# Performance work log

Hardware: AMD Instinct MI355X
Metric: run time of the kernel (lower is better)

Reference implementation:

```python
import jax, jax.numpy as jnp
import numpy as np
from jax import lax

C = 512
BN_EPS = 1e-5
GLN_EPS = 1e-8


def setup_inputs() -> dict:
    key = jax.random.key(0)
    ks = jax.random.split(key, 10)
    B, T = 16, 4000
    x = jax.random.normal(ks[0], (B, C, T), dtype=jnp.float32)
    # BatchNorm1d params (eval mode: affine + running stats)
    bn_gamma = jax.random.normal(ks[1], (C,), dtype=jnp.float32) * 0.1 + 1.0
    bn_beta = jax.random.normal(ks[2], (C,), dtype=jnp.float32) * 0.1
    bn_mean = jax.random.normal(ks[3], (C,), dtype=jnp.float32) * 0.1
    bn_var = jax.random.uniform(ks[4], (C,), dtype=jnp.float32) + 0.5
    # depthwise Conv1d(512,512,3,groups=512,bias=False): kernel [O=C, I=1, K=3]
    dw_w = jax.random.normal(ks[5], (C, 1, 3), dtype=jnp.float32) * (1.0 / np.sqrt(3.0))
    # PReLU default: single shared parameter init 0.25
    prelu_a = jnp.full((1,), 0.25, dtype=jnp.float32)
    # GlobalLayerNorm(512) affine params
    gln_gamma = jnp.ones((C,), dtype=jnp.float32)
    gln_beta = jnp.zeros((C,), dtype=jnp.float32)
    # pointwise Conv1d(512,512,1,bias=False): weight [O, I]
    pw_w = jax.random.normal(ks[6], (C, C), dtype=jnp.float32) * (1.0 / np.sqrt(C))
    return {"x": x, "bn_gamma": bn_gamma, "bn_beta": bn_beta, "bn_mean": bn_mean,
            "bn_var": bn_var, "dw_w": dw_w, "prelu_a": prelu_a,
            "gln_gamma": gln_gamma, "gln_beta": gln_beta, "pw_w": pw_w}


def reference(x, bn_gamma, bn_beta, bn_mean, bn_var, dw_w, prelu_a,
              gln_gamma, gln_beta, pw_w):
    # ReLU
    h = jax.nn.relu(x)
    # BatchNorm1d (eval mode, running stats), per-channel affine over [B,C,T]
    scale = (bn_gamma * lax.rsqrt(bn_var + BN_EPS))[None, :, None]
    h = h * scale + (bn_beta - bn_mean * bn_gamma * lax.rsqrt(bn_var + BN_EPS))[None, :, None]
    # depthwise conv1d, kernel 3, pad 1, groups=C
    h = lax.conv_general_dilated(h, dw_w, window_strides=(1,), padding=((1, 1),),
                                 feature_group_count=C,
                                 dimension_numbers=("NCH", "OIH", "NCH"))
    # PReLU (single shared slope)
    h = jnp.where(h >= 0, h, prelu_a[0] * h)
    # GlobalLayerNorm: normalize over (C, T) per sample, per-channel affine
    mean = jnp.mean(h, axis=(1, 2), keepdims=True)
    var = jnp.mean(jnp.square(h - mean), axis=(1, 2), keepdims=True)
    h = gln_gamma[None, :, None] * (h - mean) * lax.rsqrt(var + GLN_EPS) + gln_beta[None, :, None]
    # pointwise 1x1 conv == channel GEMM
    h = jnp.einsum("oc,bct->bot", pw_w, h)
    # residual
    return h + x
```

## Files before the change

kernel.cpp:

```cpp
#include <hip/hip_runtime.h>
#include <stdint.h>

#define B_ 16
#define C_ 512
#define T_ 4000
#define TPAD 4096

typedef float f32x4 __attribute__((ext_vector_type(4)));
typedef __bf16 bf16x8 __attribute__((ext_vector_type(8)));

__device__ inline unsigned short f2b(float f) {
  uint32_t u = __builtin_bit_cast(uint32_t, f);
  u = (u + 0x7fffu + ((u >> 16) & 1u)) >> 16;
  return (unsigned short)u;
}
__device__ inline float b2f(unsigned short h) {
  uint32_t u = ((uint32_t)h) << 16;
  return __builtin_bit_cast(float, u);
}
__device__ inline void gl_lds16(const void* g, void* s) {
  __builtin_amdgcn_global_load_lds(
      (const __attribute__((address_space(1))) uint32_t*)g,
      (__attribute__((address_space(3))) uint32_t*)s, 16, 0, 0);
}


__global__ void k_init(float* wsf) {
  int i = threadIdx.x;
  if (i < 32) wsf[i] = 0.f;
}

__global__ __launch_bounds__(64) void k_prepw(const float* __restrict__ pw,
                                              const float* __restrict__ gamma,
                                              const float* __restrict__ beta,
                                              unsigned short* __restrict__ Wp,
                                              float* __restrict__ wsf) {
  int o = blockIdx.x, l = threadIdx.x;
  float a1 = 0.f, a2 = 0.f;
  for (int j = 0; j < 8; ++j) {
    int c = j * 64 + l;
    float wv = pw[o * 512 + c];
    unsigned short wb = f2b(wv * gamma[c]);
    Wp[o * 512 + c] = wb;
    a1 += b2f(wb);
    a2 += wv * beta[c];
  }
  for (int s = 32; s > 0; s >>= 1) { a1 += __shfl_down(a1, s); a2 += __shfl_down(a2, s); }
  if (l == 0) { wsf[64 + o] = a1; wsf[576 + o] = a2; }
}

__global__ __launch_bounds__(512) void k_front(const float* __restrict__ x,
    const float* __restrict__ bng, const float* __restrict__ bnb,
    const float* __restrict__ bnm, const float* __restrict__ bnv,
    const float* __restrict__ dw, const float* __restrict__ pa,
    unsigned short* __restrict__ hT, float* __restrict__ wsf) {
  __shared__ unsigned short hs[256 * 128] __attribute__((aligned(16)));
  __shared__ float psc[128], pbi[128], pq0[128], pq1[128], pq2[128];
  __shared__ float partial[16];
  int tid = threadIdx.x;
  int l = tid & 63, w = tid >> 6;
  int tb = blockIdx.x;
  int cb = blockIdx.y;
  int b  = blockIdx.z;
  int t0 = tb * 256;
  if (tid < 128) {
    int c = cb * 128 + tid;
    float sc = bng[c] * rsqrtf(bnv[c] + 1e-5f);
    psc[tid] = sc;
    pbi[tid] = bnb[c] - bnm[c] * sc;
    pq0[tid] = dw[3 * c];
    pq1[tid] = dw[3 * c + 1];
    pq2[tid] = dw[3 * c + 2];
  }
  float alpha = pa[0];
  __syncthreads();

  int t = t0 + 4 * l;
  bool full = (t + 3 < T_);
  bool has_l = (t0 > 0);
  bool has_r = (t0 + 256 < T_);
  float sum = 0.f, sq = 0.f;
  int cs_x = (l & 7) << 3;

#pragma unroll 2
  for (int i = 0; i < 16; ++i) {
    int cl = w * 16 + i;
    const float* xr = x + ((size_t)b * C_ + cb * 128 + cl) * T_;
    float sc = psc[cl], bi = pbi[cl];
    float w0 = pq0[cl], w1 = pq1[cl], w2 = pq2[cl];
    f32x4 u;
    if (full) {
      const f32x4 v = *(const f32x4*)(xr + t);
      u.x = fmaxf(v.x, 0.f) * sc + bi;
      u.y = fmaxf(v.y, 0.f) * sc + bi;
      u.z = fmaxf(v.z, 0.f) * sc + bi;
      u.w = fmaxf(v.w, 0.f) * sc + bi;
    } else {
      u = (f32x4){0.f, 0.f, 0.f, 0.f};
    }
    float el = has_l ? (fmaxf(xr[t0 - 1], 0.f) * sc + bi) : 0.f;
    float er = has_r ? (fmaxf(xr[t0 + 256], 0.f) * sc + bi) : 0.f;
    float up = __shfl_up(u.w, 1);   if (l == 0)  up = el;
    float un = __shfl_down(u.x, 1); if (l == 63) un = er;
    float h[4];
    h[0] = w0 * up  + w1 * u.x + w2 * u.y;
    h[1] = w0 * u.x + w1 * u.y + w2 * u.z;
    h[2] = w0 * u.y + w1 * u.z + w2 * u.w;
    h[3] = w0 * u.z + w1 * u.w + w2 * un;
    int cs = cl ^ cs_x;
#pragma unroll
    for (int j = 0; j < 4; ++j) {
      float p = h[j] >= 0.f ? h[j] : alpha * h[j];
      if (!full) p = 0.f;
      sum += p; sq += p * p;
      hs[(4 * l + j) * 128 + cs] = f2b(p);
    }
  }

  for (int s = 32; s > 0; s >>= 1) { sum += __shfl_down(sum, s); sq += __shfl_down(sq, s); }
  if (l == 0) { partial[w] = sum; partial[8 + w] = sq; }
  __syncthreads();
  if (tid == 0) {
    float a = 0.f, c2 = 0.f;
    for (int k = 0; k < 8; ++k) { a += partial[k]; c2 += partial[8 + k]; }
    atomicAdd(&wsf[b], a);
    atomicAdd(&wsf[16 + b], c2);
  }

  unsigned short* dstb = hT + ((size_t)b * TPAD + t0) * 512 + cb * 128;
#pragma unroll
  for (int p = 0; p < 8; ++p) {
    int idx = p * 512 + tid;
    int tl = idx >> 4, g = idx & 15;
    int gs = g ^ ((tl >> 2) & 7);
    uint4 val = *(const uint4*)(hs + tl * 128 + gs * 8);
    *(uint4*)(dstb + (size_t)tl * 512 + g * 8) = val;
  }
}

__global__ void k_finalize(float* wsf) {
  int b = threadIdx.x;
  if (b < 16) {
    float n = (float)C_ * (float)T_;
    float mean = wsf[b] / n;
    float var = wsf[16 + b] / n - mean * mean;
    wsf[32 + b] = mean;
    wsf[48 + b] = rsqrtf(fmaxf(var, 0.f) + 1e-8f);
  }
}

__global__ __launch_bounds__(256) void k_gemm(const unsigned short* __restrict__ Wp,
    const unsigned short* __restrict__ hT, const float* __restrict__ x,
    const float* __restrict__ wsf, float* __restrict__ out) {
  __shared__ unsigned short As[128 * 64];
  __shared__ unsigned short Bs[128 * 64];
  int tid = threadIdx.x;
  int l = tid & 63, w = tid >> 6;
  int nb = blockIdx.x, mb = blockIdx.y, b = blockIdx.z;
  int wm = w >> 1, wn = w & 1;
  const unsigned short* hTb = hT + (size_t)b * TPAD * 512;

  int aoff[4], boff[4];
#pragma unroll
  for (int r = 0; r < 4; ++r) {
    int i = r * 256 + tid;
    int row = i >> 3, s = i & 7;
    int ksl = (s ^ (row & 7)) << 3;
    aoff[r] = (mb * 128 + row) * 512 + ksl;
    boff[r] = (nb * 128 + row) * 512 + ksl;
  }

  f32x4 acc[4][4] = {};
  for (int ks = 0; ks < 8; ++ks) {
    int kofs = ks * 64;
#pragma unroll
    for (int r = 0; r < 4; ++r) {
      int i = r * 256 + tid;
      gl_lds16(Wp + aoff[r] + kofs, As + i * 8);
      gl_lds16(hTb + boff[r] + kofs, Bs + i * 8);
    }
    __syncthreads();
#pragma unroll
    for (int kk = 0; kk < 2; ++kk) {
      bf16x8 af[4], bfr[4];
#pragma unroll
      for (int fm = 0; fm < 4; ++fm) {
        int row = wm * 64 + fm * 16 + (l & 15);
        int slot = ((l >> 4) + kk * 4) ^ (row & 7);
        af[fm] = *(const bf16x8*)(As + row * 64 + slot * 8);
      }
#pragma unroll
      for (int fn = 0; fn < 4; ++fn) {
        int row = wn * 64 + fn * 16 + (l & 15);
        int slot = ((l >> 4) + kk * 4) ^ (row & 7);
        bfr[fn] = *(const bf16x8*)(Bs + row * 64 + slot * 8);
      }
#pragma unroll
      for (int fm = 0; fm < 4; ++fm)
#pragma unroll
        for (int fn = 0; fn < 4; ++fn)
          acc[fm][fn] = __builtin_amdgcn_mfma_f32_16x16x32_bf16(af[fm], bfr[fn], acc[fm][fn], 0, 0, 0);
    }
    __syncthreads();
  }

  float mean = wsf[32 + b], rstd = wsf[48 + b];
  float mr = mean * rstd;
#pragma unroll
  for (int fm = 0; fm < 4; ++fm) {
    int o0 = mb * 128 + wm * 64 + fm * 16 + ((l >> 4) << 2);
    float bias[4];
#pragma unroll
    for (int j = 0; j < 4; ++j) {
      int o = o0 + j;
      bias[j] = wsf[576 + o] - mr * wsf[64 + o];
    }
#pragma unroll
    for (int fn = 0; fn < 4; ++fn) {
      int t = nb * 128 + wn * 64 + fn * 16 + (l & 15);
      if (t < T_) {
#pragma unroll
        for (int j = 0; j < 4; ++j) {
          int o = o0 + j;
          size_t idx = ((size_t)b * C_ + o) * T_ + t;
          out[idx] = rstd * acc[fm][fn][j] + bias[j] + x[idx];
        }
      }
    }
  }
}

extern "C" void kernel_launch(void* const* d_in, const int* in_sizes, int n_in,
                              void* d_out, int out_size, void* d_ws, size_t ws_size,
                              hipStream_t stream) {
  const float* x   = (const float*)d_in[0];
  const float* bng = (const float*)d_in[1];
  const float* bnb = (const float*)d_in[2];
  const float* bnm = (const float*)d_in[3];
  const float* bnv = (const float*)d_in[4];
  const float* dw  = (const float*)d_in[5];
  const float* pa  = (const float*)d_in[6];
  const float* gg  = (const float*)d_in[7];
  const float* gb  = (const float*)d_in[8];
  const float* pw  = (const float*)d_in[9];
  float* out = (float*)d_out;
  float* wsf = (float*)d_ws;
  unsigned short* Wp = (unsigned short*)((char*)d_ws + 8192);
  unsigned short* hT = (unsigned short*)((char*)d_ws + (1 << 20));

  k_init<<<dim3(1), dim3(64), 0, stream>>>(wsf);
  k_prepw<<<dim3(512), dim3(64), 0, stream>>>(pw, gg, gb, Wp, wsf);
  k_front<<<dim3(16, 4, 16), dim3(512), 0, stream>>>(x, bng, bnb, bnm, bnv, dw, pa, hT, wsf);
  k_finalize<<<dim3(1), dim3(64), 0, stream>>>(wsf);
  k_gemm<<<dim3(32, 4, 16), dim3(256), 0, stream>>>(Wp, hT, x, wsf, out);
}
```

Baseline: 156.4 us.

## Double-buffer GEMM LDS tiles with 256x256 blocks and 8 waves

After: 153.9 us. No clear change (-1.6%).

```diff
diff --git a/kernel.cpp b/kernel.cpp
--- a/kernel.cpp
+++ b/kernel.cpp
@@ -149,66 +149,84 @@
   }
 }
 
-__global__ __launch_bounds__(256) void k_gemm(const unsigned short* __restrict__ Wp,
+__global__ __launch_bounds__(512, 2) void k_gemm(const unsigned short* __restrict__ Wp,
     const unsigned short* __restrict__ hT, const float* __restrict__ x,
     const float* __restrict__ wsf, float* __restrict__ out) {
-  __shared__ unsigned short As[128 * 64];
-  __shared__ unsigned short Bs[128 * 64];
+  __shared__ unsigned short As0[8192], As1[8192], Bs0[8192], Bs1[8192];
   int tid = threadIdx.x;
   int l = tid & 63, w = tid >> 6;
   int nb = blockIdx.x, mb = blockIdx.y, b = blockIdx.z;
-  int wm = w >> 1, wn = w & 1;
+  int wm = w >> 2, wn = w & 3;
   const unsigned short* hTb = hT + (size_t)b * TPAD * 512;
 
-  int aoff[4], boff[4];
-#pragma unroll
-  for (int r = 0; r < 4; ++r) {
-    int i = r * 256 + tid;
-    int row = i >> 3, s = i & 7;
-    int ksl = (s ^ (row & 7)) << 3;
-    aoff[r] = (mb * 128 + row) * 512 + ksl;
-    boff[r] = (nb * 128 + row) * 512 + ksl;
-  }
-
-  f32x4 acc[4][4] = {};
-  for (int ks = 0; ks < 8; ++ks) {
-    int kofs = ks * 64;
-#pragma unroll
-    for (int r = 0; r < 4; ++r) {
-      int i = r * 256 + tid;
-      gl_lds16(Wp + aoff[r] + kofs, As + i * 8);
-      gl_lds16(hTb + boff[r] + kofs, Bs + i * 8);
-    }
+  int aoff[2], boff[2], ldso[2];
+#pragma unroll
+  for (int r = 0; r < 2; ++r) {
+    int i = r * 512 + tid;
+    int row = i >> 2, s = i & 3;
+    int ksl = (s ^ ((row >> 1) & 3)) << 3;
+    aoff[r] = (mb * 256 + row) * 512 + ksl;
+    boff[r] = (nb * 256 + row) * 512 + ksl;
+    ldso[r] = i * 8;
+  }
+
+  int aro[8], bro[4];
+#pragma unroll
+  for (int fm = 0; fm < 8; ++fm) {
+    int row = wm * 128 + fm * 16 + (l & 15);
+    int slot = (l >> 4) ^ ((row >> 1) & 3);
+    aro[fm] = row * 32 + slot * 8;
+  }
+#pragma unroll
+  for (int fn = 0; fn < 4; ++fn) {
+    int row = wn * 64 + fn * 16 + (l & 15);
+    int slot = (l >> 4) ^ ((row >> 1) & 3);
+    bro[fn] = row * 32 + slot * 8;
+  }
+
+  const unsigned short *cA = As0, *cB = Bs0;
+  unsigned short *nA = As1, *nB = Bs1;
+
+#pragma unroll
+  for (int r = 0; r < 2; ++r) {
+    gl_lds16(Wp + aoff[r], As0 + ldso[r]);
+    gl_lds16(hTb + boff[r], Bs0 + ldso[r]);
+  }
+  __syncthreads();
+
+  f32x4 acc[8][4] = {};
+#pragma unroll 1
+  for (int kt = 0; kt < 16; ++kt) {
+    if (kt < 15) {
+      int kofs = (kt + 1) * 32;
+#pragma unroll
+      for (int r = 0; r < 2; ++r) {
+        gl_lds16(Wp + aoff[r] + kofs, nA + ldso[r]);
+        gl_lds16(hTb + boff[r] + kofs, nB + ldso[r]);
+      }
+    }
+    bf16x8 af[8], bfv[4];
+#pragma unroll
+    for (int fm = 0; fm < 8; ++fm) af[fm] = *(const bf16x8*)(cA + aro[fm]);
+#pragma unroll
+    for (int fn = 0; fn < 4; ++fn) bfv[fn] = *(const bf16x8*)(cB + bro[fn]);
+    __builtin_amdgcn_s_setprio(1);
+#pragma unroll
+    for (int fm = 0; fm < 8; ++fm)
+#pragma unroll
+      for (int fn = 0; fn < 4; ++fn)
+        acc[fm][fn] = __builtin_amdgcn_mfma_f32_16x16x32_bf16(af[fm], bfv[fn], acc[fm][fn], 0, 0, 0);
+    __builtin_amdgcn_s_setprio(0);
     __syncthreads();
-#pragma unroll
-    for (int kk = 0; kk < 2; ++kk) {
-      bf16x8 af[4], bfr[4];
-#pragma unroll
-      for (int fm = 0; fm < 4; ++fm) {
-        int row = wm * 64 + fm * 16 + (l & 15);
-        int slot = ((l >> 4) + kk * 4) ^ (row & 7);
-        af[fm] = *(const bf16x8*)(As + row * 64 + slot * 8);
-      }
-#pragma unroll
-      for (int fn = 0; fn < 4; ++fn) {
-        int row = wn * 64 + fn * 16 + (l & 15);
-        int slot = ((l >> 4) + kk * 4) ^ (row & 7);
-        bfr[fn] = *(const bf16x8*)(Bs + row * 64 + slot * 8);
-      }
-#pragma unroll
-      for (int fm = 0; fm < 4; ++fm)
-#pragma unroll
-        for (int fn = 0; fn < 4; ++fn)
-          acc[fm][fn] = __builtin_amdgcn_mfma_f32_16x16x32_bf16(af[fm], bfr[fn], acc[fm][fn], 0, 0, 0);
-    }
-    __syncthreads();
+    const unsigned short* t1 = cA; cA = nA; nA = (unsigned short*)t1;
+    const unsigned short* t2 = cB; cB = nB; nB = (unsigned short*)t2;
   }
 
   float mean = wsf[32 + b], rstd = wsf[48 + b];
   float mr = mean * rstd;
 #pragma unroll
-  for (int fm = 0; fm < 4; ++fm) {
-    int o0 = mb * 128 + wm * 64 + fm * 16 + ((l >> 4) << 2);
+  for (int fm = 0; fm < 8; ++fm) {
+    int o0 = mb * 256 + wm * 128 + fm * 16 + ((l >> 4) << 2);
     float bias[4];
 #pragma unroll
     for (int j = 0; j < 4; ++j) {
@@ -217,7 +235,7 @@
     }
 #pragma unroll
     for (int fn = 0; fn < 4; ++fn) {
-      int t = nb * 128 + wn * 64 + fn * 16 + (l & 15);
+      int t = nb * 256 + wn * 64 + fn * 16 + (l & 15);
       if (t < T_) {
 #pragma unroll
         for (int j = 0; j < 4; ++j) {
@@ -252,5 +270,5 @@
   k_prepw<<<dim3(512), dim3(64), 0, stream>>>(pw, gg, gb, Wp, wsf);
   k_front<<<dim3(16, 4, 16), dim3(512), 0, stream>>>(x, bng, bnb, bnm, bnv, dw, pa, hT, wsf);
   k_finalize<<<dim3(1), dim3(64), 0, stream>>>(wsf);
-  k_gemm<<<dim3(32, 4, 16), dim3(256), 0, stream>>>(Wp, hT, x, wsf, out);
-}
+  k_gemm<<<dim3(16, 2, 16), dim3(512), 0, stream>>>(Wp, hT, x, wsf, out);
+}
```

## Restructure GEMM to full-M blocks with B tile resident in LDS and 32x32 MFMA

Applied to the files above, without the earlier changes.

Measured after the change: 188.6 us. +20.5%, slower.

```diff
diff --git a/kernel.cpp b/kernel.cpp
--- a/kernel.cpp
+++ b/kernel.cpp
@@ -7,6 +7,7 @@
 #define TPAD 4096
 
 typedef float f32x4 __attribute__((ext_vector_type(4)));
+typedef float f32x16 __attribute__((ext_vector_type(16)));
 typedef __bf16 bf16x8 __attribute__((ext_vector_type(8)));
 
 __device__ inline unsigned short f2b(float f) {
@@ -149,81 +150,103 @@
   }
 }
 
-__global__ __launch_bounds__(256) void k_gemm(const unsigned short* __restrict__ Wp,
+__global__ __launch_bounds__(512, 4) void k_gemm(const unsigned short* __restrict__ Wp,
     const unsigned short* __restrict__ hT, const float* __restrict__ x,
     const float* __restrict__ wsf, float* __restrict__ out) {
-  __shared__ unsigned short As[128 * 64];
-  __shared__ unsigned short Bs[128 * 64];
+  __shared__ unsigned short Bs[64 * 512] __attribute__((aligned(16)));
   int tid = threadIdx.x;
   int l = tid & 63, w = tid >> 6;
-  int nb = blockIdx.x, mb = blockIdx.y, b = blockIdx.z;
-  int wm = w >> 1, wn = w & 1;
-  const unsigned short* hTb = hT + (size_t)b * TPAD * 512;
-
-  int aoff[4], boff[4];
-#pragma unroll
-  for (int r = 0; r < 4; ++r) {
-    int i = r * 256 + tid;
-    int row = i >> 3, s = i & 7;
-    int ksl = (s ^ (row & 7)) << 3;
-    aoff[r] = (mb * 128 + row) * 512 + ksl;
-    boff[r] = (nb * 128 + row) * 512 + ksl;
-  }
-
-  f32x4 acc[4][4] = {};
-  for (int ks = 0; ks < 8; ++ks) {
-    int kofs = ks * 64;
-#pragma unroll
-    for (int r = 0; r < 4; ++r) {
-      int i = r * 256 + tid;
-      gl_lds16(Wp + aoff[r] + kofs, As + i * 8);
-      gl_lds16(hTb + boff[r] + kofs, Bs + i * 8);
-    }
-    __syncthreads();
-#pragma unroll
-    for (int kk = 0; kk < 2; ++kk) {
-      bf16x8 af[4], bfr[4];
-#pragma unroll
-      for (int fm = 0; fm < 4; ++fm) {
-        int row = wm * 64 + fm * 16 + (l & 15);
-        int slot = ((l >> 4) + kk * 4) ^ (row & 7);
-        af[fm] = *(const bf16x8*)(As + row * 64 + slot * 8);
-      }
-#pragma unroll
-      for (int fn = 0; fn < 4; ++fn) {
-        int row = wn * 64 + fn * 16 + (l & 15);
-        int slot = ((l >> 4) + kk * 4) ^ (row & 7);
-        bfr[fn] = *(const bf16x8*)(Bs + row * 64 + slot * 8);
-      }
-#pragma unroll
-      for (int fm = 0; fm < 4; ++fm)
-#pragma unroll
-        for (int fn = 0; fn < 4; ++fn)
-          acc[fm][fn] = __builtin_amdgcn_mfma_f32_16x16x32_bf16(af[fm], bfr[fn], acc[fm][fn], 0, 0, 0);
-    }
-    __syncthreads();
+  int nb = blockIdx.x, b = blockIdx.y;
+  const unsigned short* hTt = hT + ((size_t)b * TPAD + nb * 64) * 512;
+
+#pragma unroll
+  for (int r = 0; r < 8; ++r) {
+    int u = r * 512 + tid;
+    int row = u >> 6, slot = u & 63;
+    gl_lds16(hTt + row * 512 + ((slot ^ (row & 31)) << 3), Bs + u * 8);
+  }
+  asm volatile("s_waitcnt vmcnt(0)" ::: "memory");
+  __syncthreads();
+
+  int o0 = w * 64;
+  int lr = l & 31, lh = l >> 5;
+  const unsigned short* wpb = Wp + (size_t)(o0 + lr) * 512 + lh * 8;
+  const unsigned short* bs0 = Bs + lr * 512;
+
+  f32x16 acc[2][2] = {};
+  bf16x8 A0[2][2], A1[2][2];
+#pragma unroll
+  for (int fm = 0; fm < 2; ++fm)
+#pragma unroll
+    for (int ks = 0; ks < 2; ++ks)
+      A0[fm][ks] = *(const bf16x8*)(wpb + fm * 32 * 512 + ks * 16);
+
+#pragma unroll 1
+  for (int kt = 0; kt < 16; kt += 2) {
+#pragma unroll
+    for (int fm = 0; fm < 2; ++fm)
+#pragma unroll
+      for (int ks = 0; ks < 2; ++ks)
+        A1[fm][ks] = *(const bf16x8*)(wpb + fm * 32 * 512 + (kt + 1) * 32 + ks * 16);
+    {
+      bf16x8 bv[2][2];
+#pragma unroll
+      for (int fn = 0; fn < 2; ++fn)
+#pragma unroll
+        for (int ks = 0; ks < 2; ++ks) {
+          int slot = (kt * 4 + ks * 2 + lh) ^ lr;
+          bv[fn][ks] = *(const bf16x8*)(bs0 + fn * 32 * 512 + slot * 8);
+        }
+#pragma unroll
+      for (int ks = 0; ks < 2; ++ks)
+#pragma unroll
+        for (int fm = 0; fm < 2; ++fm)
+#pragma unroll
+          for (int fn = 0; fn < 2; ++fn)
+            acc[fm][fn] = __builtin_amdgcn_mfma_f32_32x32x16_bf16(
+                A0[fm][ks], bv[fn][ks], acc[fm][fn], 0, 0, 0);
+    }
+    if (kt + 2 < 16) {
+#pragma unroll
+      for (int fm = 0; fm < 2; ++fm)
+#pragma unroll
+        for (int ks = 0; ks < 2; ++ks)
+          A0[fm][ks] = *(const bf16x8*)(wpb + fm * 32 * 512 + (kt + 2) * 32 + ks * 16);
+    }
+    {
+      bf16x8 bv[2][2];
+#pragma unroll
+      for (int fn = 0; fn < 2; ++fn)
+#pragma unroll
+        for (int ks = 0; ks < 2; ++ks) {
+          int slot = ((kt + 1) * 4 + ks * 2 + lh) ^ lr;
+          bv[fn][ks] = *(const bf16x8*)(bs0 + fn * 32 * 512 + slot * 8);
+        }
+#pragma unroll
+      for (int ks = 0; ks < 2; ++ks)
+#pragma unroll
+        for (int fm = 0; fm < 2; ++fm)
+#pragma unroll
+          for (int fn = 0; fn < 2; ++fn)
+            acc[fm][fn] = __builtin_amdgcn_mfma_f32_32x32x16_bf16(
+                A1[fm][ks], bv[fn][ks], acc[fm][fn], 0, 0, 0);
+    }
   }
 
   float mean = wsf[32 + b], rstd = wsf[48 + b];
   float mr = mean * rstd;
 #pragma unroll
-  for (int fm = 0; fm < 4; ++fm) {
-    int o0 = mb * 128 + wm * 64 + fm * 16 + ((l >> 4) << 2);
-    float bias[4];
-#pragma unroll
-    for (int j = 0; j < 4; ++j) {
-      int o = o0 + j;
-      bias[j] = wsf[576 + o] - mr * wsf[64 + o];
-    }
-#pragma unroll
-    for (int fn = 0; fn < 4; ++fn) {
-      int t = nb * 128 + wn * 64 + fn * 16 + (l & 15);
+  for (int fm = 0; fm < 2; ++fm) {
+#pragma unroll
+    for (int fn = 0; fn < 2; ++fn) {
+      int t = nb * 64 + fn * 32 + lr;
       if (t < T_) {
 #pragma unroll
-        for (int j = 0; j < 4; ++j) {
-          int o = o0 + j;
+        for (int reg = 0; reg < 16; ++reg) {
+          int o = o0 + fm * 32 + (reg & 3) + ((reg >> 2) << 3) + (lh << 2);
+          float bias = wsf[576 + o] - mr * wsf[64 + o];
           size_t idx = ((size_t)b * C_ + o) * T_ + t;
-          out[idx] = rstd * acc[fm][fn][j] + bias[j] + x[idx];
+          out[idx] = rstd * acc[fm][fn][reg] + bias + x[idx];
         }
       }
     }
@@ -252,5 +275,5 @@
   k_prepw<<<dim3(512), dim3(64), 0, stream>>>(pw, gg, gb, Wp, wsf);
   k_front<<<dim3(16, 4, 16), dim3(512), 0, stream>>>(x, bng, bnb, bnm, bnv, dw, pa, hT, wsf);
   k_finalize<<<dim3(1), dim3(64), 0, stream>>>(wsf);
-  k_gemm<<<dim3(32, 4, 16), dim3(256), 0, stream>>>(Wp, hT, x, wsf, out);
-}
+  k_gemm<<<dim3(64, 16), dim3(512), 0, stream>>>(Wp, hT, x, wsf, out);
+}
```

## Keep weight tile in registers and double-buffer hT tiles in GEMM

Applied to the files above, without the earlier changes.

Result: slower. 207.0 us (+32.4%).

```diff
diff --git a/kernel.cpp b/kernel.cpp
--- a/kernel.cpp
+++ b/kernel.cpp
@@ -7,6 +7,7 @@
 #define TPAD 4096
 
 typedef float f32x4 __attribute__((ext_vector_type(4)));
+typedef float f32x16 __attribute__((ext_vector_type(16)));
 typedef __bf16 bf16x8 __attribute__((ext_vector_type(8)));
 
 __device__ inline unsigned short f2b(float f) {
@@ -41,7 +42,7 @@
     int c = j * 64 + l;
     float wv = pw[o * 512 + c];
     unsigned short wb = f2b(wv * gamma[c]);
-    Wp[o * 512 + c] = wb;
+    Wp[((size_t)(c >> 3) * 512 + o) * 8 + (c & 7)] = wb;
     a1 += b2f(wb);
     a2 += wv * beta[c];
   }
@@ -149,84 +150,79 @@
   }
 }
 
-__global__ __launch_bounds__(256) void k_gemm(const unsigned short* __restrict__ Wp,
+#define STAGE(it, buf) do {                                                   \
+  _Pragma("unroll")                                                           \
+  for (int r_ = 0; r_ < 4; ++r_) {                                            \
+    int u_ = r_ * 512 + tid;                                                  \
+    int row_ = u_ >> 6, slot_ = u_ & 63;                                      \
+    gl_lds16(hTb + (size_t)((it) * 32 + row_) * 512 + ((slot_ ^ row_) << 3),  \
+             (buf) + u_ * 8);                                                 \
+  } } while (0)
+
+__global__ __launch_bounds__(512, 2) void k_gemm(const unsigned short* __restrict__ Wp,
     const unsigned short* __restrict__ hT, const float* __restrict__ x,
     const float* __restrict__ wsf, float* __restrict__ out) {
-  __shared__ unsigned short As[128 * 64];
-  __shared__ unsigned short Bs[128 * 64];
+  __shared__ unsigned short Bs0[32 * 512] __attribute__((aligned(16)));
+  __shared__ unsigned short Bs1[32 * 512] __attribute__((aligned(16)));
   int tid = threadIdx.x;
   int l = tid & 63, w = tid >> 6;
-  int nb = blockIdx.x, mb = blockIdx.y, b = blockIdx.z;
-  int wm = w >> 1, wn = w & 1;
-  const unsigned short* hTb = hT + (size_t)b * TPAD * 512;
-
-  int aoff[4], boff[4];
-#pragma unroll
-  for (int r = 0; r < 4; ++r) {
-    int i = r * 256 + tid;
-    int row = i >> 3, s = i & 7;
-    int ksl = (s ^ (row & 7)) << 3;
-    aoff[r] = (mb * 128 + row) * 512 + ksl;
-    boff[r] = (nb * 128 + row) * 512 + ksl;
-  }
-
-  f32x4 acc[4][4] = {};
-  for (int ks = 0; ks < 8; ++ks) {
-    int kofs = ks * 64;
-#pragma unroll
-    for (int r = 0; r < 4; ++r) {
-      int i = r * 256 + tid;
-      gl_lds16(Wp + aoff[r] + kofs, As + i * 8);
-      gl_lds16(hTb + boff[r] + kofs, Bs + i * 8);
-    }
-    __syncthreads();
-#pragma unroll
-    for (int kk = 0; kk < 2; ++kk) {
-      bf16x8 af[4], bfr[4];
-#pragma unroll
-      for (int fm = 0; fm < 4; ++fm) {
-        int row = wm * 64 + fm * 16 + (l & 15);
-        int slot = ((l >> 4) + kk * 4) ^ (row & 7);
-        af[fm] = *(const bf16x8*)(As + row * 64 + slot * 8);
+  int lr = l & 31, lh = l >> 5;
+  int bid = blockIdx.x;
+  int mb = bid & 1, b = (bid >> 1) & 15, tg = bid >> 5;
+  int o0w = mb * 256 + w * 32;
+  const unsigned short* hTb = hT + ((size_t)b * TPAD + tg * 512) * 512;
+
+  bf16x8 Areg[32];
+#pragma unroll
+  for (int kc = 0; kc < 32; ++kc)
+    Areg[kc] = *(const bf16x8*)(Wp + ((size_t)(kc * 2 + lh) * 512 + o0w + lr) * 8);
+
+  STAGE(0, Bs0);
+  STAGE(1, Bs1);
+  asm volatile("s_waitcnt vmcnt(4)" ::: "memory");
+  __builtin_amdgcn_s_barrier();
+  __builtin_amdgcn_sched_barrier(0);
+
+  float rstd = wsf[48 + b], mean = wsf[32 + b];
+  float mr = mean * rstd;
+  float bias[16];
+#pragma unroll
+  for (int reg = 0; reg < 16; ++reg) {
+    int o = o0w + (reg & 3) + ((reg >> 2) << 3) + (lh << 2);
+    bias[reg] = wsf[576 + o] - mr * wsf[64 + o];
+  }
+
+#pragma unroll 1
+  for (int it = 0; it < 16; ++it) {
+    unsigned short* cur = (it & 1) ? Bs1 : Bs0;
+    f32x16 acc = {};
+#pragma unroll
+    for (int kc = 0; kc < 32; ++kc) {
+      int slot = (kc * 2 + lh) ^ lr;
+      bf16x8 bv = *(const bf16x8*)(cur + lr * 512 + slot * 8);
+      acc = __builtin_amdgcn_mfma_f32_32x32x16_bf16(Areg[kc], bv, acc, 0, 0, 0);
+    }
+    asm volatile("s_waitcnt lgkmcnt(0)" ::: "memory");
+    __builtin_amdgcn_s_barrier();
+    __builtin_amdgcn_sched_barrier(0);
+    if (it < 14) {
+      STAGE(it + 2, cur);
+      asm volatile("s_waitcnt vmcnt(4)" ::: "memory");
+    } else {
+      asm volatile("s_waitcnt vmcnt(0)" ::: "memory");
+    }
+    __builtin_amdgcn_sched_barrier(0);
+    int t = tg * 512 + it * 32 + lr;
+    if (t < T_) {
+#pragma unroll
+      for (int reg = 0; reg < 16; ++reg) {
+        int o = o0w + (reg & 3) + ((reg >> 2) << 3) + (lh << 2);
+        size_t idx = ((size_t)b * C_ + o) * T_ + t;
+        out[idx] = rstd * acc[reg] + bias[reg] + x[idx];
       }
-#pragma unroll
-      for (int fn = 0; fn < 4; ++fn) {
-        int row = wn * 64 + fn * 16 + (l & 15);
-        int slot = ((l >> 4) + kk * 4) ^ (row & 7);
-        bfr[fn] = *(const bf16x8*)(Bs + row * 64 + slot * 8);
-      }
-#pragma unroll
-      for (int fm = 0; fm < 4; ++fm)
-#pragma unroll
-        for (int fn = 0; fn < 4; ++fn)
-          acc[fm][fn] = __builtin_amdgcn_mfma_f32_16x16x32_bf16(af[fm], bfr[fn], acc[fm][fn], 0, 0, 0);
-    }
-    __syncthreads();
-  }
-
-  float mean = wsf[32 + b], rstd = wsf[48 + b];
-  float mr = mean * rstd;
-#pragma unroll
-  for (int fm = 0; fm < 4; ++fm) {
-    int o0 = mb * 128 + wm * 64 + fm * 16 + ((l >> 4) << 2);
-    float bias[4];
-#pragma unroll
-    for (int j = 0; j < 4; ++j) {
-      int o = o0 + j;
-      bias[j] = wsf[576 + o] - mr * wsf[64 + o];
-    }
-#pragma unroll
-    for (int fn = 0; fn < 4; ++fn) {
-      int t = nb * 128 + wn * 64 + fn * 16 + (l & 15);
-      if (t < T_) {
-#pragma unroll
-        for (int j = 0; j < 4; ++j) {
-          int o = o0 + j;
-          size_t idx = ((size_t)b * C_ + o) * T_ + t;
-          out[idx] = rstd * acc[fm][fn][j] + bias[j] + x[idx];
-        }
-      }
-    }
+    }
+    __builtin_amdgcn_s_barrier();
+    __builtin_amdgcn_sched_barrier(0);
   }
 }
 
@@ -252,5 +248,5 @@
   k_prepw<<<dim3(512), dim3(64), 0, stream>>>(pw, gg, gb, Wp, wsf);
   k_front<<<dim3(16, 4, 16), dim3(512), 0, stream>>>(x, bng, bnb, bnm, bnv, dw, pa, hT, wsf);
   k_finalize<<<dim3(1), dim3(64), 0, stream>>>(wsf);
-  k_gemm<<<dim3(32, 4, 16), dim3(256), 0, stream>>>(Wp, hT, x, wsf, out);
-}
+  k_gemm<<<dim3(256), dim3(512), 0, stream>>>(Wp, hT, x, wsf, out);
+}
```
